# Kernel tuning notes

Hardware: AMD Instinct MI355X
Metric: run time of the kernel (lower is better)

Reference implementation:

```python
import jax, jax.numpy as jnp
import numpy as np
import math

B, T, C = 4, 2048, 1024
H = 16
D = C // H  # head_dim = 64

def setup_inputs() -> dict:
    key = jax.random.key(0)
    k1, k2, k3 = jax.random.split(key, 3)
    x = jax.random.normal(k1, (B, T, C), dtype=jnp.float32)
    # weights stored as [in, out]; torch Linear weight is [out,in], applied as x @ W^T
    w_qkv = jax.random.normal(k2, (C, 3 * C), dtype=jnp.float32) * (1.0 / math.sqrt(C))
    w_proj = jax.random.normal(k3, (C, C), dtype=jnp.float32) * (1.0 / math.sqrt(C))
    return {"x": x, "w_qkv": w_qkv, "w_proj": w_proj}

def reference(x, w_qkv, w_proj):
    qkv = x @ w_qkv                                   # [B,T,3C]
    q, k, v = jnp.split(qkv, 3, axis=-1)
    # [B,T,C] -> [B,H,T,D]
    q = q.reshape(B, T, H, D).transpose(0, 2, 1, 3)
    k = k.reshape(B, T, H, D).transpose(0, 2, 1, 3)
    v = v.reshape(B, T, H, D).transpose(0, 2, 1, 3)
    scale = 1.0 / math.sqrt(D)
    att = jnp.einsum('bhqd,bhkd->bhqk', q, k) * scale  # [B,H,T,T]
    causal = jnp.tril(jnp.ones((T, T), dtype=bool))
    att = jnp.where(causal[None, None, :, :], att, jnp.float32(-jnp.inf))
    att = jax.nn.softmax(att, axis=-1)
    y = jnp.einsum('bhqk,bhkd->bhqd', att, v)          # [B,H,T,D]
    y = y.transpose(0, 2, 1, 3).reshape(B, T, C)
    return y @ w_proj
```

## Files before the change

### kernel.cpp

```cpp
#include <hip/hip_runtime.h>
#include <hip/hip_bf16.h>
#include <stdint.h>

typedef __attribute__((ext_vector_type(4))) float f32x4;
typedef __attribute__((ext_vector_type(8))) short bf16x8;
typedef __attribute__((ext_vector_type(2))) unsigned uint2v;

constexpr int BATCH = 4;
constexpr int SEQ   = 2048;
constexpr int CDIM  = 1024;
constexpr int NH    = 16;
constexpr int DH    = 64;
constexpr int MROWS = BATCH * SEQ;

__device__ __forceinline__ unsigned short f2bf(float f) {
  unsigned int u = __float_as_uint(f);
  u += 0x7FFFu + ((u >> 16) & 1u);
  return (unsigned short)(u >> 16);
}

__device__ __forceinline__ void gload16(const void* g, void* l) {
  __builtin_amdgcn_global_load_lds(
      (const __attribute__((address_space(1))) void*)g,
      (__attribute__((address_space(3))) void*)l, 16, 0, 0);
}

__device__ __forceinline__ unsigned cvtpk_bf16(float lo, float hi) {
  unsigned r;
  asm("v_cvt_pk_bf16_f32 %0, %1, %2" : "=v"(r) : "v"(lo), "v"(hi));
  return r;
}
__device__ __forceinline__ float crossmax4(float v) {
  uint2v r = __builtin_amdgcn_permlane32_swap(__float_as_uint(v), __float_as_uint(v), false, false);
  float m = fmaxf(__uint_as_float(r[0]), __uint_as_float(r[1]));
  uint2v r2 = __builtin_amdgcn_permlane16_swap(__float_as_uint(m), __float_as_uint(m), false, false);
  return fmaxf(__uint_as_float(r2[0]), __uint_as_float(r2[1]));
}
__device__ __forceinline__ float crosssum4(float v) {
  uint2v r = __builtin_amdgcn_permlane32_swap(__float_as_uint(v), __float_as_uint(v), false, false);
  float m = __uint_as_float(r[0]) + __uint_as_float(r[1]);
  uint2v r2 = __builtin_amdgcn_permlane16_swap(__float_as_uint(m), __float_as_uint(m), false, false);
  return __uint_as_float(r2[0]) + __uint_as_float(r2[1]);
}

__global__ __launch_bounds__(256) void k_cvt(const float* __restrict__ in,
                                             unsigned short* __restrict__ out, int n4) {
  int i = blockIdx.x * blockDim.x + threadIdx.x;
  int stride = gridDim.x * blockDim.x;
  for (; i < n4; i += stride) {
    float4 v = reinterpret_cast<const float4*>(in)[i];
    ushort4 o;
    o.x = f2bf(v.x); o.y = f2bf(v.y); o.z = f2bf(v.z); o.w = f2bf(v.w);
    reinterpret_cast<ushort4*>(out)[i] = o;
  }
}

__global__ __launch_bounds__(256) void k_tcvt(const float* __restrict__ in,
                                              unsigned short* __restrict__ out, int K, int N) {
  __shared__ float tile[32][33];
  int n0 = blockIdx.x * 32, k0 = blockIdx.y * 32;
  int tx = threadIdx.x, ty = threadIdx.y;
#pragma unroll
  for (int r = 0; r < 32; r += 8)
    tile[ty + r][tx] = in[(size_t)(k0 + ty + r) * N + n0 + tx];
  __syncthreads();
#pragma unroll
  for (int r = 0; r < 32; r += 8)
    out[(size_t)(n0 + ty + r) * K + k0 + tx] = f2bf(tile[tx][ty + r]);
}

template <int EPI>
__global__ __launch_bounds__(256) void k_gemm_bt(const unsigned short* __restrict__ A,
                                                 const unsigned short* __restrict__ Bt,
                                                 int M, int N, int K,
                                                 unsigned short* __restrict__ outQ,
                                                 unsigned short* __restrict__ outK,
                                                 unsigned short* __restrict__ outVt,
                                                 float* __restrict__ outC) {
  constexpr int BM = 128, BN = 128, BK = 64;
  __shared__ __align__(16) unsigned short smem[BM * BK * 2];
  unsigned short* As = smem;
  unsigned short* Bs = smem + BM * BK;
  const int nbn = N / BN;
  const int cpx = (nbn * (M / BM)) >> 3;
  const int orig = blockIdx.x;
  const int work = (orig & 7) * cpx + (orig >> 3);
  const int bn = work % nbn, bm = work / nbn;
  const int tid = threadIdx.x;
  const int lane = tid & 63, wave = tid >> 6;
  const int wm = wave >> 1, wn = wave & 1;
  const int l15 = lane & 15, l4 = lane >> 4;

  f32x4 acc[4][4];
#pragma unroll
  for (int i = 0; i < 4; ++i)
#pragma unroll
    for (int j = 0; j < 4; ++j) acc[i][j] = f32x4{0.f, 0.f, 0.f, 0.f};

  const int grow = lane >> 3;
  const int chL  = lane & 7;
  const int nk = K / BK;

  for (int kt = 0; kt < nk; ++kt) {
    __syncthreads();
#pragma unroll
    for (int c = 0; c < 4; ++c) {
      int row = wave * 32 + c * 8 + grow;
      int cg = chL ^ (row & 7);
      gload16(A + (size_t)(bm * BM + row) * K + kt * BK + cg * 8,
              reinterpret_cast<char*>(As) + (wave * 32 + c * 8) * 128);
      gload16(Bt + (size_t)(bn * BN + row) * K + kt * BK + cg * 8,
              reinterpret_cast<char*>(Bs) + (wave * 32 + c * 8) * 128);
    }
    asm volatile("s_waitcnt vmcnt(0)" ::: "memory");
    __syncthreads();
#pragma unroll
    for (int s = 0; s < 2; ++s) {
      bf16x8 af[4], bfr[4];
#pragma unroll
      for (int i = 0; i < 4; ++i) {
        int row = wm * 64 + i * 16 + l15;
        int off = row * 128 + ((s * 64 + l4 * 16) ^ ((row & 7) << 4));
        af[i] = *reinterpret_cast<const bf16x8*>(reinterpret_cast<char*>(As) + off);
      }
#pragma unroll
      for (int j = 0; j < 4; ++j) {
        int row = wn * 64 + j * 16 + l15;
        int off = row * 128 + ((s * 64 + l4 * 16) ^ ((row & 7) << 4));
        bfr[j] = *reinterpret_cast<const bf16x8*>(reinterpret_cast<char*>(Bs) + off);
      }
      __builtin_amdgcn_s_setprio(1);
#pragma unroll
      for (int i = 0; i < 4; ++i)
#pragma unroll
        for (int j = 0; j < 4; ++j)
          acc[i][j] = __builtin_amdgcn_mfma_f32_16x16x32_bf16(af[i], bfr[j], acc[i][j], 0, 0, 0);
      __builtin_amdgcn_s_setprio(0);
    }
  }

  if (EPI == 0) {
    const int sel = (bn * BN) >> 10;
    const float qsc = (sel == 0) ? 0.18033688f : 1.0f;
    char* stg = reinterpret_cast<char*>(smem);
    __syncthreads();
    const int b = (bm * BM) >> 11, tbase = (bm * BM) & 2047;
    if (sel < 2) {
#pragma unroll
      for (int i = 0; i < 4; ++i) {
        int wr = wm * 64 + i * 16 + l4 * 4;
#pragma unroll
        for (int j = 0; j < 4; ++j) {
          int wc = wn * 64 + j * 16 + l15;
#pragma unroll
          for (int r = 0; r < 4; ++r) {
            int row = wr + r;
            int off = row * 256 + ((wc * 2) ^ (((row >> 2) & 7) << 4));
            *reinterpret_cast<unsigned short*>(stg + off) = f2bf(acc[i][j][r] * qsc);
          }
        }
      }
      __syncthreads();
      unsigned short* dst = (sel == 0) ? outQ : outK;
#pragma unroll
      for (int ii = 0; ii < 8; ++ii) {
        int chunk = ii * 256 + tid;
        int row = chunk >> 4, ch = chunk & 15;
        int off = row * 256 + ((ch * 16) ^ (((row >> 2) & 7) << 4));
        uint4 ld = *reinterpret_cast<const uint4*>(stg + off);
        int n = bn * BN + ch * 8;
        int c = n & 1023, h = c >> 6, d = c & 63;
        *reinterpret_cast<uint4*>(dst + ((size_t)(b * NH + h) * SEQ + tbase + row) * DH + d) = ld;
      }
    } else {
#pragma unroll
      for (int i = 0; i < 4; ++i) {
        int wr = wm * 64 + i * 16 + l4 * 4;
#pragma unroll
        for (int j = 0; j < 4; ++j) {
          int wc = wn * 64 + j * 16 + l15;
          ushort4 pw;
          pw.x = f2bf(acc[i][j][0]); pw.y = f2bf(acc[i][j][1]);
          pw.z = f2bf(acc[i][j][2]); pw.w = f2bf(acc[i][j][3]);
          int off = wc * 256 + ((wr * 2) ^ ((wc & 7) << 4));
          *reinterpret_cast<ushort4*>(stg + off) = pw;
        }
      }
      __syncthreads();
#pragma unroll
      for (int ii = 0; ii < 8; ++ii) {
        int chunk = ii * 256 + tid;
        int col = chunk >> 4, tch = chunk & 15;
        int off = col * 256 + ((tch * 16) ^ ((col & 7) << 4));
        uint4 ld = *reinterpret_cast<const uint4*>(stg + off);
        int n = bn * BN + col;
        int c = n & 1023, h = c >> 6, d = c & 63;
        *reinterpret_cast<uint4*>(outVt + ((size_t)(b * NH + h) * DH + d) * SEQ + tbase + tch * 8) = ld;
      }
    }
  } else {
#pragma unroll
    for (int i = 0; i < 4; ++i) {
      int mbase = bm * BM + wm * 64 + i * 16 + l4 * 4;
#pragma unroll
      for (int j = 0; j < 4; ++j) {
        int n = bn * BN + wn * 64 + j * 16 + l15;
#pragma unroll
        for (int r = 0; r < 4; ++r)
          outC[(size_t)(mbase + r) * N + n] = acc[i][j][r];
      }
    }
  }
}

template <bool MASK>
__device__ __forceinline__ void attn_step(const unsigned short* __restrict__ Ksb,
                                          const unsigned short* __restrict__ Vsb,
                                          const bf16x8 (&qf)[2], f32x4 (&oacc)[4],
                                          float& mrun, float& lrun,
                                          int kb, int q, int l15, int l4) {
  f32x4 sac[4];
#pragma unroll
  for (int mf = 0; mf < 4; ++mf) {
    sac[mf] = f32x4{0.f, 0.f, 0.f, 0.f};
#pragma unroll
    for (int s = 0; s < 2; ++s) {
      int row = mf * 16 + l15;
      int off = row * 128 + ((s * 64 + l4 * 16) ^ ((row & 7) << 4));
      bf16x8 kf = *reinterpret_cast<const bf16x8*>(reinterpret_cast<const char*>(Ksb) + off);
      __builtin_amdgcn_s_setprio(1);
      sac[mf] = __builtin_amdgcn_mfma_f32_16x16x32_bf16(kf, qf[s], sac[mf], 0, 0, 0);
      __builtin_amdgcn_s_setprio(0);
    }
  }
  float tm = -1e30f;
#pragma unroll
  for (int mf = 0; mf < 4; ++mf)
#pragma unroll
    for (int r = 0; r < 4; ++r) {
      float x = sac[mf][r];
      if (MASK) {
        int key = kb + mf * 16 + l4 * 4 + r;
        if (key > q) x = -1e30f;
      }
      sac[mf][r] = x;
      tm = fmaxf(tm, x);
    }
  tm = crossmax4(tm);
  if (__any(tm > mrun + 8.f)) {
    float mnew = fmaxf(mrun, tm);
    float corr = __builtin_amdgcn_exp2f(mrun - mnew);
    lrun *= corr;
#pragma unroll
    for (int mf = 0; mf < 4; ++mf) {
      oacc[mf][0] *= corr; oacc[mf][1] *= corr;
      oacc[mf][2] *= corr; oacc[mf][3] *= corr;
    }
    mrun = mnew;
  }
  float ts = 0.f;
#pragma unroll
  for (int mf = 0; mf < 4; ++mf)
#pragma unroll
    for (int r = 0; r < 4; ++r) {
      float e = __builtin_amdgcn_exp2f(sac[mf][r] - mrun);
      sac[mf][r] = e;
      ts += e;
    }
  lrun += crosssum4(ts);
  bf16x8 pf[2];
#pragma unroll
  for (int s = 0; s < 2; ++s) {
    unsigned a0 = cvtpk_bf16(sac[2 * s][0], sac[2 * s][1]);
    unsigned a1 = cvtpk_bf16(sac[2 * s][2], sac[2 * s][3]);
    unsigned b0 = cvtpk_bf16(sac[2 * s + 1][0], sac[2 * s + 1][1]);
    unsigned b1 = cvtpk_bf16(sac[2 * s + 1][2], sac[2 * s + 1][3]);
    uint2v r0 = __builtin_amdgcn_permlane32_swap(a0, b0, false, false);
    uint2v r1 = __builtin_amdgcn_permlane32_swap(a1, b1, false, false);
    uint2v q0 = __builtin_amdgcn_permlane16_swap(r0[0], r0[1], false, false);
    uint2v q1 = __builtin_amdgcn_permlane16_swap(r1[0], r1[1], false, false);
    union { unsigned u[4]; bf16x8 v; } t;
    t.u[0] = q0[0]; t.u[1] = q1[0]; t.u[2] = q0[1]; t.u[3] = q1[1];
    pf[s] = t.v;
  }
#pragma unroll
  for (int mf = 0; mf < 4; ++mf) {
#pragma unroll
    for (int s = 0; s < 2; ++s) {
      int row = mf * 16 + l15;
      int off = row * 128 + ((s * 64 + l4 * 16) ^ ((row & 7) << 4));
      bf16x8 vf = *reinterpret_cast<const bf16x8*>(reinterpret_cast<const char*>(Vsb) + off);
      __builtin_amdgcn_s_setprio(1);
      oacc[mf] = __builtin_amdgcn_mfma_f32_16x16x32_bf16(vf, pf[s], oacc[mf], 0, 0, 0);
      __builtin_amdgcn_s_setprio(0);
    }
  }
}

__global__ __launch_bounds__(512, 8) void k_attn(const unsigned short* __restrict__ Qg,
                                                 const unsigned short* __restrict__ Kg,
                                                 const unsigned short* __restrict__ Vtg,
                                                 unsigned short* __restrict__ Yg) {
  __shared__ __align__(16) unsigned short K3[3][64 * 64];
  __shared__ __align__(16) unsigned short V2[2][64 * 64];

  const int orig = blockIdx.x;
  const int work = (orig & 7) * 128 + (orig >> 3);
  const int jb = work & 15;
  const int bh = work >> 4;
  const int h = bh & (NH - 1), b = bh >> 4;
  const int tid = threadIdx.x;
  const int lane = tid & 63, wave = tid >> 6;
  const int l15 = lane & 15, l4 = lane >> 4;
  const int wgrp = wave >> 2, wsub = wave & 3;

  const int qtB = 31 - jb;
  const int myqt = wgrp ? jb : qtB;
  const int q = myqt * 64 + wsub * 16 + l15;

  bf16x8 qf[2];
#pragma unroll
  for (int s = 0; s < 2; ++s)
    qf[s] = *reinterpret_cast<const bf16x8*>(Qg + ((size_t)bh * SEQ + q) * DH + s * 32 + l4 * 8);

  f32x4 oacc[4];
#pragma unroll
  for (int mf = 0; mf < 4; ++mf) oacc[mf] = f32x4{0.f, 0.f, 0.f, 0.f};
  float mrun = -1e30f, lrun = 0.f;

  const int srow = wave * 8 + (lane >> 3);
  const int scg  = (lane & 7) ^ (srow & 7);
  const size_t kbg = (size_t)bh * SEQ * DH;
  const size_t vbg = (size_t)bh * DH * SEQ;

  gload16(Kg + kbg + (size_t)srow * DH + scg * 8,
          reinterpret_cast<char*>(&K3[0][0]) + wave * 1024);
  gload16(Kg + kbg + (size_t)(64 + srow) * DH + scg * 8,
          reinterpret_cast<char*>(&K3[1][0]) + wave * 1024);
  gload16(Vtg + vbg + (size_t)srow * SEQ + scg * 8,
          reinterpret_cast<char*>(&V2[0][0]) + wave * 1024);
  asm volatile("s_waitcnt vmcnt(0)" ::: "memory");
  __syncthreads();

  int kcur = 0;
  int k2dst = 2;
  for (int kt = 0; kt <= qtB; ++kt) {
    if (kt + 1 <= qtB)
      gload16(Vtg + vbg + (size_t)srow * SEQ + (kt + 1) * 64 + scg * 8,
              reinterpret_cast<char*>(&V2[(kt + 1) & 1][0]) + wave * 1024);
    if (kt + 2 <= qtB)
      gload16(Kg + kbg + (size_t)((kt + 2) * 64 + srow) * DH + scg * 8,
              reinterpret_cast<char*>(&K3[k2dst][0]) + wave * 1024);
    if (kt <= myqt) {
      const unsigned short* Kc = &K3[kcur][0];
      const unsigned short* Vc = &V2[kt & 1][0];
      if (kt == myqt) attn_step<true>(Kc, Vc, qf, oacc, mrun, lrun, kt * 64, q, l15, l4);
      else            attn_step<false>(Kc, Vc, qf, oacc, mrun, lrun, kt * 64, q, l15, l4);
    }
    if (kt + 2 <= qtB) asm volatile("s_waitcnt vmcnt(1)" ::: "memory");
    else               asm volatile("s_waitcnt vmcnt(0)" ::: "memory");
    __builtin_amdgcn_sched_barrier(0);
    __builtin_amdgcn_s_barrier();
    kcur = (kcur == 2) ? 0 : kcur + 1;
    k2dst = (k2dst == 2) ? 0 : k2dst + 1;
  }

  const float inv = 1.f / lrun;
  char* stg = reinterpret_cast<char*>(&K3[0][0]) + wave * 2048;
#pragma unroll
  for (int mf = 0; mf < 4; ++mf) {
    ushort4 ov;
    ov.x = f2bf(oacc[mf][0] * inv); ov.y = f2bf(oacc[mf][1] * inv);
    ov.z = f2bf(oacc[mf][2] * inv); ov.w = f2bf(oacc[mf][3] * inv);
    int off = l15 * 128 + ((mf * 32 + l4 * 8) ^ ((l15 & 7) << 4));
    *reinterpret_cast<ushort4*>(stg + off) = ov;
  }
  const int qbase = myqt * 64 + wsub * 16;
#pragma unroll
  for (int ii = 0; ii < 2; ++ii) {
    int c = ii * 64 + lane;
    int row = c >> 3, ch = c & 7;
    int off = row * 128 + ((ch * 16) ^ ((row & 7) << 4));
    uint4 ld = *reinterpret_cast<const uint4*>(stg + off);
    *reinterpret_cast<uint4*>(Yg + (size_t)(b * SEQ + qbase + row) * CDIM + h * 64 + ch * 8) = ld;
  }
}

extern "C" void kernel_launch(void* const* d_in, const int* in_sizes, int n_in,
                              void* d_out, int out_size, void* d_ws, size_t ws_size,
                              hipStream_t stream) {
  const float* x      = (const float*)d_in[0];
  const float* w_qkv  = (const float*)d_in[1];
  const float* w_proj = (const float*)d_in[2];
  float* out = (float*)d_out;
  char* ws = (char*)d_ws;

  unsigned short* Xb  = (unsigned short*)(ws);
  unsigned short* WqT = (unsigned short*)(ws + (size_t)16777216);
  unsigned short* WpT = (unsigned short*)(ws + (size_t)23068672);
  unsigned short* Q   = (unsigned short*)(ws + (size_t)25165824);
  unsigned short* K   = (unsigned short*)(ws + (size_t)41943040);
  unsigned short* Vt  = (unsigned short*)(ws + (size_t)58720256);
  unsigned short* Y   = Xb;

  k_cvt<<<2048, 256, 0, stream>>>(x, Xb, (BATCH * SEQ * CDIM) / 4);
  k_tcvt<<<dim3((3 * CDIM) / 32, CDIM / 32), dim3(32, 8), 0, stream>>>(w_qkv, WqT, CDIM, 3 * CDIM);
  k_tcvt<<<dim3(CDIM / 32, CDIM / 32), dim3(32, 8), 0, stream>>>(w_proj, WpT, CDIM, CDIM);

  k_gemm_bt<0><<<1536, 256, 0, stream>>>(
      Xb, WqT, MROWS, 3 * CDIM, CDIM, Q, K, Vt, nullptr);

  k_attn<<<1024, 512, 0, stream>>>(Q, K, Vt, Y);

  k_gemm_bt<1><<<512, 256, 0, stream>>>(
      Y, WpT, MROWS, CDIM, CDIM, nullptr, nullptr, nullptr, out);
}
```

Before: 160.5 us.

## Have each attention wave process both paired query tiles, sharing K/V fragment loads

The attention block drops from 8 waves to 4. Each wave now handles 16 rows from both the long and the short query tile of a causal pair, so every K and V fragment read from shared memory feeds two MFMAs. Before, the two wave groups read the same data separately and the short-tile group sat idle after its diagonal. Staging now issues two loads per wave per tile to fill the shared buffers. The cost is higher register pressure from doubled accumulators and fewer waves per block to hide latency.

New measurement: 166.9 us. 4.0% more time.

```diff
diff --git a/kernel.cpp b/kernel.cpp
--- a/kernel.cpp
+++ b/kernel.cpp
@@ -213,75 +213,130 @@
   }
 }
 
-template <bool MASK>
-__device__ __forceinline__ void attn_step(const unsigned short* __restrict__ Ksb,
+template <bool MASKL, bool DOS, bool MASKS>
+__device__ __forceinline__ void step_dual(const unsigned short* __restrict__ Ksb,
                                           const unsigned short* __restrict__ Vsb,
-                                          const bf16x8 (&qf)[2], f32x4 (&oacc)[4],
-                                          float& mrun, float& lrun,
-                                          int kb, int q, int l15, int l4) {
-  f32x4 sac[4];
+                                          const bf16x8 (&qfL)[2], const bf16x8 (&qfS)[2],
+                                          f32x4 (&oaccL)[4], f32x4 (&oaccS)[4],
+                                          float& mL, float& lL, float& mS, float& lS,
+                                          int kb, int qL, int qS, int l15, int l4) {
+  f32x4 sacL[4], sacS[4];
 #pragma unroll
   for (int mf = 0; mf < 4; ++mf) {
-    sac[mf] = f32x4{0.f, 0.f, 0.f, 0.f};
+    sacL[mf] = f32x4{0.f, 0.f, 0.f, 0.f};
+    if (DOS) sacS[mf] = f32x4{0.f, 0.f, 0.f, 0.f};
 #pragma unroll
     for (int s = 0; s < 2; ++s) {
       int row = mf * 16 + l15;
       int off = row * 128 + ((s * 64 + l4 * 16) ^ ((row & 7) << 4));
       bf16x8 kf = *reinterpret_cast<const bf16x8*>(reinterpret_cast<const char*>(Ksb) + off);
       __builtin_amdgcn_s_setprio(1);
-      sac[mf] = __builtin_amdgcn_mfma_f32_16x16x32_bf16(kf, qf[s], sac[mf], 0, 0, 0);
+      sacL[mf] = __builtin_amdgcn_mfma_f32_16x16x32_bf16(kf, qfL[s], sacL[mf], 0, 0, 0);
+      if (DOS) sacS[mf] = __builtin_amdgcn_mfma_f32_16x16x32_bf16(kf, qfS[s], sacS[mf], 0, 0, 0);
       __builtin_amdgcn_s_setprio(0);
     }
   }
-  float tm = -1e30f;
+  float tmL = -1e30f, tmS = -1e30f;
 #pragma unroll
   for (int mf = 0; mf < 4; ++mf)
 #pragma unroll
     for (int r = 0; r < 4; ++r) {
-      float x = sac[mf][r];
-      if (MASK) {
+      float x = sacL[mf][r];
+      if (MASKL) {
         int key = kb + mf * 16 + l4 * 4 + r;
-        if (key > q) x = -1e30f;
-      }
-      sac[mf][r] = x;
-      tm = fmaxf(tm, x);
-    }
-  tm = crossmax4(tm);
-  if (__any(tm > mrun + 8.f)) {
-    float mnew = fmaxf(mrun, tm);
-    float corr = __builtin_amdgcn_exp2f(mrun - mnew);
-    lrun *= corr;
+        if (key > qL) x = -1e30f;
+      }
+      sacL[mf][r] = x;
+      tmL = fmaxf(tmL, x);
+    }
+  if (DOS) {
+#pragma unroll
+    for (int mf = 0; mf < 4; ++mf)
+#pragma unroll
+      for (int r = 0; r < 4; ++r) {
+        float x = sacS[mf][r];
+        if (MASKS) {
+          int key = kb + mf * 16 + l4 * 4 + r;
+          if (key > qS) x = -1e30f;
+        }
+        sacS[mf][r] = x;
+        tmS = fmaxf(tmS, x);
+      }
+  }
+  tmL = crossmax4(tmL);
+  if (DOS) tmS = crossmax4(tmS);
+  if (__any(tmL > mL + 8.f)) {
+    float mnew = fmaxf(mL, tmL);
+    float corr = __builtin_amdgcn_exp2f(mL - mnew);
+    lL *= corr;
 #pragma unroll
     for (int mf = 0; mf < 4; ++mf) {
-      oacc[mf][0] *= corr; oacc[mf][1] *= corr;
-      oacc[mf][2] *= corr; oacc[mf][3] *= corr;
-    }
-    mrun = mnew;
-  }
-  float ts = 0.f;
+      oaccL[mf][0] *= corr; oaccL[mf][1] *= corr;
+      oaccL[mf][2] *= corr; oaccL[mf][3] *= corr;
+    }
+    mL = mnew;
+  }
+  if (DOS && __any(tmS > mS + 8.f)) {
+    float mnew = fmaxf(mS, tmS);
+    float corr = __builtin_amdgcn_exp2f(mS - mnew);
+    lS *= corr;
+#pragma unroll
+    for (int mf = 0; mf < 4; ++mf) {
+      oaccS[mf][0] *= corr; oaccS[mf][1] *= corr;
+      oaccS[mf][2] *= corr; oaccS[mf][3] *= corr;
+    }
+    mS = mnew;
+  }
+  float tsL = 0.f, tsS = 0.f;
 #pragma unroll
   for (int mf = 0; mf < 4; ++mf)
 #pragma unroll
     for (int r = 0; r < 4; ++r) {
-      float e = __builtin_amdgcn_exp2f(sac[mf][r] - mrun);
-      sac[mf][r] = e;
-      ts += e;
-    }
-  lrun += crosssum4(ts);
-  bf16x8 pf[2];
+      float e = __builtin_amdgcn_exp2f(sacL[mf][r] - mL);
+      sacL[mf][r] = e;
+      tsL += e;
+    }
+  if (DOS) {
+#pragma unroll
+    for (int mf = 0; mf < 4; ++mf)
+#pragma unroll
+      for (int r = 0; r < 4; ++r) {
+        float e = __builtin_amdgcn_exp2f(sacS[mf][r] - mS);
+        sacS[mf][r] = e;
+        tsS += e;
+      }
+  }
+  lL += crosssum4(tsL);
+  if (DOS) lS += crosssum4(tsS);
+  bf16x8 pfL[2], pfS[2];
 #pragma unroll
   for (int s = 0; s < 2; ++s) {
-    unsigned a0 = cvtpk_bf16(sac[2 * s][0], sac[2 * s][1]);
-    unsigned a1 = cvtpk_bf16(sac[2 * s][2], sac[2 * s][3]);
-    unsigned b0 = cvtpk_bf16(sac[2 * s + 1][0], sac[2 * s + 1][1]);
-    unsigned b1 = cvtpk_bf16(sac[2 * s + 1][2], sac[2 * s + 1][3]);
-    uint2v r0 = __builtin_amdgcn_permlane32_swap(a0, b0, false, false);
-    uint2v r1 = __builtin_amdgcn_permlane32_swap(a1, b1, false, false);
-    uint2v q0 = __builtin_amdgcn_permlane16_swap(r0[0], r0[1], false, false);
-    uint2v q1 = __builtin_amdgcn_permlane16_swap(r1[0], r1[1], false, false);
-    union { unsigned u[4]; bf16x8 v; } t;
-    t.u[0] = q0[0]; t.u[1] = q1[0]; t.u[2] = q0[1]; t.u[3] = q1[1];
-    pf[s] = t.v;
+    {
+      unsigned a0 = cvtpk_bf16(sacL[2 * s][0], sacL[2 * s][1]);
+      unsigned a1 = cvtpk_bf16(sacL[2 * s][2], sacL[2 * s][3]);
+      unsigned b0 = cvtpk_bf16(sacL[2 * s + 1][0], sacL[2 * s + 1][1]);
+      unsigned b1 = cvtpk_bf16(sacL[2 * s + 1][2], sacL[2 * s + 1][3]);
+      uint2v r0 = __builtin_amdgcn_permlane32_swap(a0, b0, false, false);
+      uint2v r1 = __builtin_amdgcn_permlane32_swap(a1, b1, false, false);
+      uint2v q0 = __builtin_amdgcn_permlane16_swap(r0[0], r0[1], false, false);
+      uint2v q1 = __builtin_amdgcn_permlane16_swap(r1[0], r1[1], false, false);
+      union { unsigned u[4]; bf16x8 v; } t;
+      t.u[0] = q0[0]; t.u[1] = q1[0]; t.u[2] = q0[1]; t.u[3] = q1[1];
+      pfL[s] = t.v;
+    }
+    if (DOS) {
+      unsigned a0 = cvtpk_bf16(sacS[2 * s][0], sacS[2 * s][1]);
+      unsigned a1 = cvtpk_bf16(sacS[2 * s][2], sacS[2 * s][3]);
+      unsigned b0 = cvtpk_bf16(sacS[2 * s + 1][0], sacS[2 * s + 1][1]);
+      unsigned b1 = cvtpk_bf16(sacS[2 * s + 1][2], sacS[2 * s + 1][3]);
+      uint2v r0 = __builtin_amdgcn_permlane32_swap(a0, b0, false, false);
+      uint2v r1 = __builtin_amdgcn_permlane32_swap(a1, b1, false, false);
+      uint2v q0 = __builtin_amdgcn_permlane16_swap(r0[0], r0[1], false, false);
+      uint2v q1 = __builtin_amdgcn_permlane16_swap(r1[0], r1[1], false, false);
+      union { unsigned u[4]; bf16x8 v; } t;
+      t.u[0] = q0[0]; t.u[1] = q1[0]; t.u[2] = q0[1]; t.u[3] = q1[1];
+      pfS[s] = t.v;
+    }
   }
 #pragma unroll
   for (int mf = 0; mf < 4; ++mf) {
@@ -291,13 +346,14 @@
       int off = row * 128 + ((s * 64 + l4 * 16) ^ ((row & 7) << 4));
       bf16x8 vf = *reinterpret_cast<const bf16x8*>(reinterpret_cast<const char*>(Vsb) + off);
       __builtin_amdgcn_s_setprio(1);
-      oacc[mf] = __builtin_amdgcn_mfma_f32_16x16x32_bf16(vf, pf[s], oacc[mf], 0, 0, 0);
+      oaccL[mf] = __builtin_amdgcn_mfma_f32_16x16x32_bf16(vf, pfL[s], oaccL[mf], 0, 0, 0);
+      if (DOS) oaccS[mf] = __builtin_amdgcn_mfma_f32_16x16x32_bf16(vf, pfS[s], oaccS[mf], 0, 0, 0);
       __builtin_amdgcn_s_setprio(0);
     }
   }
 }
 
-__global__ __launch_bounds__(512, 8) void k_attn(const unsigned short* __restrict__ Qg,
+__global__ __launch_bounds__(256, 4) void k_attn(const unsigned short* __restrict__ Qg,
                                                  const unsigned short* __restrict__ Kg,
                                                  const unsigned short* __restrict__ Vtg,
                                                  unsigned short* __restrict__ Yg) {
@@ -312,77 +368,105 @@
   const int tid = threadIdx.x;
   const int lane = tid & 63, wave = tid >> 6;
   const int l15 = lane & 15, l4 = lane >> 4;
-  const int wgrp = wave >> 2, wsub = wave & 3;
-
-  const int qtB = 31 - jb;
-  const int myqt = wgrp ? jb : qtB;
-  const int q = myqt * 64 + wsub * 16 + l15;
-
-  bf16x8 qf[2];
-#pragma unroll
-  for (int s = 0; s < 2; ++s)
-    qf[s] = *reinterpret_cast<const bf16x8*>(Qg + ((size_t)bh * SEQ + q) * DH + s * 32 + l4 * 8);
-
-  f32x4 oacc[4];
-#pragma unroll
-  for (int mf = 0; mf < 4; ++mf) oacc[mf] = f32x4{0.f, 0.f, 0.f, 0.f};
-  float mrun = -1e30f, lrun = 0.f;
-
-  const int srow = wave * 8 + (lane >> 3);
-  const int scg  = (lane & 7) ^ (srow & 7);
+
+  const int qtS = jb, qtL = 31 - jb;
+  const int qL = qtL * 64 + wave * 16 + l15;
+  const int qS = qtS * 64 + wave * 16 + l15;
+
+  bf16x8 qfL[2], qfS[2];
+#pragma unroll
+  for (int s = 0; s < 2; ++s) {
+    qfL[s] = *reinterpret_cast<const bf16x8*>(Qg + ((size_t)bh * SEQ + qL) * DH + s * 32 + l4 * 8);
+    qfS[s] = *reinterpret_cast<const bf16x8*>(Qg + ((size_t)bh * SEQ + qS) * DH + s * 32 + l4 * 8);
+  }
+
+  f32x4 oaccL[4], oaccS[4];
+#pragma unroll
+  for (int mf = 0; mf < 4; ++mf) {
+    oaccL[mf] = f32x4{0.f, 0.f, 0.f, 0.f};
+    oaccS[mf] = f32x4{0.f, 0.f, 0.f, 0.f};
+  }
+  float mL = -1e30f, lL = 0.f, mS = -1e30f, lS = 0.f;
+
+  const int srow0 = wave * 8 + (lane >> 3);
   const size_t kbg = (size_t)bh * SEQ * DH;
   const size_t vbg = (size_t)bh * DH * SEQ;
 
-  gload16(Kg + kbg + (size_t)srow * DH + scg * 8,
-          reinterpret_cast<char*>(&K3[0][0]) + wave * 1024);
-  gload16(Kg + kbg + (size_t)(64 + srow) * DH + scg * 8,
-          reinterpret_cast<char*>(&K3[1][0]) + wave * 1024);
-  gload16(Vtg + vbg + (size_t)srow * SEQ + scg * 8,
-          reinterpret_cast<char*>(&V2[0][0]) + wave * 1024);
+#define STAGE_K(ktile, buf)                                                     \
+  _Pragma("unroll")                                                             \
+  for (int c = 0; c < 2; ++c) {                                                 \
+    int row = c * 32 + srow0;                                                   \
+    int cg = (lane & 7) ^ (row & 7);                                            \
+    gload16(Kg + kbg + (size_t)((ktile) * 64 + row) * DH + cg * 8,              \
+            reinterpret_cast<char*>(&K3[buf][0]) + (c * 32 + wave * 8) * 128);  \
+  }
+#define STAGE_V(ktile, buf)                                                     \
+  _Pragma("unroll")                                                             \
+  for (int c = 0; c < 2; ++c) {                                                 \
+    int row = c * 32 + srow0;                                                   \
+    int cg = (lane & 7) ^ (row & 7);                                            \
+    gload16(Vtg + vbg + (size_t)row * SEQ + (ktile) * 64 + cg * 8,              \
+            reinterpret_cast<char*>(&V2[buf][0]) + (c * 32 + wave * 8) * 128);  \
+  }
+
+  STAGE_K(0, 0);
+  STAGE_K(1, 1);
+  STAGE_V(0, 0);
   asm volatile("s_waitcnt vmcnt(0)" ::: "memory");
   __syncthreads();
 
   int kcur = 0;
   int k2dst = 2;
-  for (int kt = 0; kt <= qtB; ++kt) {
-    if (kt + 1 <= qtB)
-      gload16(Vtg + vbg + (size_t)srow * SEQ + (kt + 1) * 64 + scg * 8,
-              reinterpret_cast<char*>(&V2[(kt + 1) & 1][0]) + wave * 1024);
-    if (kt + 2 <= qtB)
-      gload16(Kg + kbg + (size_t)((kt + 2) * 64 + srow) * DH + scg * 8,
-              reinterpret_cast<char*>(&K3[k2dst][0]) + wave * 1024);
-    if (kt <= myqt) {
+  for (int kt = 0; kt <= qtL; ++kt) {
+    if (kt + 1 <= qtL) STAGE_V(kt + 1, (kt + 1) & 1);
+    if (kt + 2 <= qtL) STAGE_K(kt + 2, k2dst);
+    {
       const unsigned short* Kc = &K3[kcur][0];
       const unsigned short* Vc = &V2[kt & 1][0];
-      if (kt == myqt) attn_step<true>(Kc, Vc, qf, oacc, mrun, lrun, kt * 64, q, l15, l4);
-      else            attn_step<false>(Kc, Vc, qf, oacc, mrun, lrun, kt * 64, q, l15, l4);
-    }
-    if (kt + 2 <= qtB) asm volatile("s_waitcnt vmcnt(1)" ::: "memory");
+      const int kb = kt * 64;
+      if (kt < qtS)
+        step_dual<false, true, false>(Kc, Vc, qfL, qfS, oaccL, oaccS, mL, lL, mS, lS, kb, qL, qS, l15, l4);
+      else if (kt == qtS)
+        step_dual<false, true, true>(Kc, Vc, qfL, qfS, oaccL, oaccS, mL, lL, mS, lS, kb, qL, qS, l15, l4);
+      else if (kt < qtL)
+        step_dual<false, false, false>(Kc, Vc, qfL, qfS, oaccL, oaccS, mL, lL, mS, lS, kb, qL, qS, l15, l4);
+      else
+        step_dual<true, false, false>(Kc, Vc, qfL, qfS, oaccL, oaccS, mL, lL, mS, lS, kb, qL, qS, l15, l4);
+    }
+    if (kt + 2 <= qtL) asm volatile("s_waitcnt vmcnt(2)" ::: "memory");
     else               asm volatile("s_waitcnt vmcnt(0)" ::: "memory");
     __builtin_amdgcn_sched_barrier(0);
     __builtin_amdgcn_s_barrier();
     kcur = (kcur == 2) ? 0 : kcur + 1;
     k2dst = (k2dst == 2) ? 0 : k2dst + 1;
   }
-
-  const float inv = 1.f / lrun;
-  char* stg = reinterpret_cast<char*>(&K3[0][0]) + wave * 2048;
-#pragma unroll
-  for (int mf = 0; mf < 4; ++mf) {
-    ushort4 ov;
-    ov.x = f2bf(oacc[mf][0] * inv); ov.y = f2bf(oacc[mf][1] * inv);
-    ov.z = f2bf(oacc[mf][2] * inv); ov.w = f2bf(oacc[mf][3] * inv);
-    int off = l15 * 128 + ((mf * 32 + l4 * 8) ^ ((l15 & 7) << 4));
-    *reinterpret_cast<ushort4*>(stg + off) = ov;
-  }
-  const int qbase = myqt * 64 + wsub * 16;
-#pragma unroll
-  for (int ii = 0; ii < 2; ++ii) {
-    int c = ii * 64 + lane;
-    int row = c >> 3, ch = c & 7;
-    int off = row * 128 + ((ch * 16) ^ ((row & 7) << 4));
-    uint4 ld = *reinterpret_cast<const uint4*>(stg + off);
-    *reinterpret_cast<uint4*>(Yg + (size_t)(b * SEQ + qbase + row) * CDIM + h * 64 + ch * 8) = ld;
+#undef STAGE_K
+#undef STAGE_V
+
+  __syncthreads();
+#pragma unroll
+  for (int item = 0; item < 2; ++item) {
+    const float inv = 1.f / (item ? lS : lL);
+    const int qt = item ? qtS : qtL;
+    char* stg = reinterpret_cast<char*>(&K3[0][0]) + (wave * 2 + item) * 2048;
+#pragma unroll
+    for (int mf = 0; mf < 4; ++mf) {
+      const f32x4 oc = item ? oaccS[mf] : oaccL[mf];
+      ushort4 ov;
+      ov.x = f2bf(oc[0] * inv); ov.y = f2bf(oc[1] * inv);
+      ov.z = f2bf(oc[2] * inv); ov.w = f2bf(oc[3] * inv);
+      int off = l15 * 128 + ((mf * 32 + l4 * 8) ^ ((l15 & 7) << 4));
+      *reinterpret_cast<ushort4*>(stg + off) = ov;
+    }
+    const int qbase = qt * 64 + wave * 16;
+#pragma unroll
+    for (int ii = 0; ii < 2; ++ii) {
+      int c = ii * 64 + lane;
+      int row = c >> 3, ch = c & 7;
+      int off = row * 128 + ((ch * 16) ^ ((row & 7) << 4));
+      uint4 ld = *reinterpret_cast<const uint4*>(stg + off);
+      *reinterpret_cast<uint4*>(Yg + (size_t)(b * SEQ + qbase + row) * CDIM + h * 64 + ch * 8) = ld;
+    }
   }
 }
 
@@ -410,7 +494,7 @@
   k_gemm_bt<0><<<1536, 256, 0, stream>>>(
       Xb, WqT, MROWS, 3 * CDIM, CDIM, Q, K, Vt, nullptr);
 
-  k_attn<<<1024, 512, 0, stream>>>(Q, K, Vt, Y);
+  k_attn<<<1024, 256, 0, stream>>>(Q, K, Vt, Y);
 
   k_gemm_bt<1><<<512, 256, 0, stream>>>(
       Y, WpT, MROWS, CDIM, CDIM, nullptr, nullptr, nullptr, out);
```
